# Kernel optimization log

Measured on AMD Instinct MI355X. Metric: run time of the kernel, lower is better.

Reference implementation:

```python
import jax, jax.numpy as jnp
import numpy as np

T = 3.0  # distillation temperature (hardcoded in AED.__init__)


def setup_inputs() -> dict:
    key = jax.random.key(0)
    ks = jax.random.split(key, 5)
    B, C = 1024, 32000
    return {
        "outputs1": jax.random.normal(ks[0], (B, C), dtype=jnp.float32),
        "outputs2": jax.random.normal(ks[1], (B, C), dtype=jnp.float32),
        "outputs3": jax.random.normal(ks[2], (B, C), dtype=jnp.float32),
        "outputs4": jax.random.normal(ks[3], (B, C), dtype=jnp.float32),
        "targets": jax.random.randint(ks[4], (B,), 0, C, dtype=jnp.int64),
    }


def reference(outputs1, outputs2, outputs3, outputs4, targets):
    # outs: [4, B, C]
    outs = jnp.stack([outputs1, outputs2, outputs3, outputs4], axis=0)
    mimic = jnp.mean(outs, axis=0)  # [B, C]
    C = outs.shape[-1]

    # Per-model CE loss: -log_softmax(logits)[target]  -> [4, B]
    logp = jax.nn.log_softmax(outs, axis=-1)
    CE = -jnp.take_along_axis(logp, targets[None, :, None], axis=2)[..., 0]

    # KD loss: KLDivLoss(reduction='mean') * T^2 = mean_c p_t*(log p_t - log p_s) * T^2
    teacher = 0.8 * outs + 0.2 * mimic[None]          # [4, B, C]
    log_s = jax.nn.log_softmax(outs / T, axis=-1)
    log_t = jax.nn.log_softmax(teacher / T, axis=-1)
    p_t = jnp.exp(log_t)
    KD = jnp.mean(p_t * (log_t - log_s), axis=-1) * (T * T)  # [4, B]

    Loss_IRM = jnp.sum(CE + KD, axis=0)  # [B]
    min_CE = jnp.min(CE, axis=0)         # argmin-based select == min

    # Deleting the target entry from each logit vector before the cosine is
    # equivalent (for dot products and norms) to zeroing that entry.
    tgt_mask = jax.nn.one_hot(targets, C, dtype=outs.dtype)  # [B, C]
    om = outs * (1.0 - tgt_mask[None])                        # [4, B, C]
    norms = jnp.sqrt(jnp.sum(om * om, axis=-1))               # [4, B]
    dots = jnp.einsum('jbc,kbc->jkb', om, om)                 # [4, 4, B]
    cos = dots / (norms[:, None, :] * norms[None, :, :])
    ju, ku = jnp.triu_indices(4, k=1)
    Loss_DAL = jnp.sum(cos[ju, ku], axis=0)  # [B], sum over 6 pairs j<k

    L = Loss_IRM + 0.7 * min_CE + 0.3 * Loss_DAL  # [B]
    return jnp.mean(L), mimic
```

## Files before the change

### kernel.cpp

```cpp
#include <hip/hip_runtime.h>
#include <math.h>


#define CCOLS 32000
#define VCOLS (CCOLS / 4)
#define BLOCK 512
#define NWAVES (BLOCK / 64)
#define NACC 26

__device__ __forceinline__ float wred(float v) {
#pragma unroll
  for (int o = 32; o > 0; o >>= 1) v += __shfl_down(v, o, 64);
  return v;
}

__global__ __launch_bounds__(BLOCK, 8) void aed_row(
    const float* __restrict__ x0, const float* __restrict__ x1,
    const float* __restrict__ x2, const float* __restrict__ x3,
    const int* __restrict__ tgt, float* __restrict__ out,
    float* __restrict__ rowloss) {
  const int b = blockIdx.x;
  const size_t off = (size_t)b * CCOLS;
  const float4* p0 = (const float4*)(x0 + off);
  const float4* p1 = (const float4*)(x1 + off);
  const float4* p2 = (const float4*)(x2 + off);
  const float4* p3 = (const float4*)(x3 + off);
  float* mim = out + 1 + off;

  float acc[NACC];
#pragma unroll
  for (int i = 0; i < NACC; ++i) acc[i] = 0.f;

  const float c1 = 0.48089835f;
  const float c08 = 0.38471868f;
  const float c02 = 0.09617967f;

  for (int v = threadIdx.x; v < VCOLS; v += BLOCK) {
    float4 A = p0[v];
    float4 B = p1[v];
    float4 Cc = p2[v];
    float4 D = p3[v];
    float a0[4] = {A.x, A.y, A.z, A.w};
    float a1[4] = {B.x, B.y, B.z, B.w};
    float a2[4] = {Cc.x, Cc.y, Cc.z, Cc.w};
    float a3[4] = {D.x, D.y, D.z, D.w};
#pragma unroll
    for (int u = 0; u < 4; ++u) {
      float y0 = a0[u], y1 = a1[u], y2 = a2[u], y3 = a3[u];
      float m = 0.25f * ((y0 + y1) + (y2 + y3));
      mim[4 * v + u] = m;
      float mm = m * c02;
#define MODEL(j, y)                                       \
  {                                                       \
    float t1 = __builtin_amdgcn_exp2f((y)*c1);            \
    acc[4 + (j)] += t1;                                   \
    acc[0 + (j)] += t1 * t1 * t1;                         \
    float e = __builtin_amdgcn_exp2f(fmaf((y), c08, mm)); \
    acc[8 + (j)] += e;                                    \
    acc[12 + (j)] = fmaf(e, m - (y), acc[12 + (j)]);      \
  }
      MODEL(0, y0)
      MODEL(1, y1)
      MODEL(2, y2)
      MODEL(3, y3)
#undef MODEL
      acc[16] = fmaf(y0, y0, acc[16]);
      acc[17] = fmaf(y1, y1, acc[17]);
      acc[18] = fmaf(y2, y2, acc[18]);
      acc[19] = fmaf(y3, y3, acc[19]);
      acc[20] = fmaf(y0, y1, acc[20]);
      acc[21] = fmaf(y0, y2, acc[21]);
      acc[22] = fmaf(y0, y3, acc[22]);
      acc[23] = fmaf(y1, y2, acc[23]);
      acc[24] = fmaf(y1, y3, acc[24]);
      acc[25] = fmaf(y2, y3, acc[25]);
    }
  }

  __shared__ float sm[NWAVES][NACC];
  const int lane = threadIdx.x & 63;
  const int wid = threadIdx.x >> 6;
#pragma unroll
  for (int i = 0; i < NACC; ++i) {
    float r = wred(acc[i]);
    if (lane == 0) sm[wid][i] = r;
  }
  __syncthreads();

  if (threadIdx.x == 0) {
    float t[NACC];
#pragma unroll
    for (int i = 0; i < NACC; ++i) {
      float s = 0.f;
#pragma unroll
      for (int w = 0; w < NWAVES; ++w) s += sm[w][i];
      t[i] = s;
    }

    const int tg = tgt[b];
    float tv[4];
    tv[0] = x0[off + tg];
    tv[1] = x1[off + tg];
    tv[2] = x2[off + tg];
    tv[3] = x3[off + tg];

    float CE[4], KD[4];
#pragma unroll
    for (int j = 0; j < 4; ++j) {
      CE[j] = logf(t[0 + j]) - tv[j];
      float LS = logf(t[4 + j]);
      float LT = logf(t[8 + j]);
      float S = t[12 + j] / t[8 + j];
      KD[j] = (9.f / 32000.f) * fmaf(0.2f / 3.f, S, LS - LT);
    }

    float n[4];
#pragma unroll
    for (int j = 0; j < 4; ++j) n[j] = sqrtf(t[16 + j] - tv[j] * tv[j]);

    float DAL = 0.f;
    DAL += (t[20] - tv[0] * tv[1]) / (n[0] * n[1]);
    DAL += (t[21] - tv[0] * tv[2]) / (n[0] * n[2]);
    DAL += (t[22] - tv[0] * tv[3]) / (n[0] * n[3]);
    DAL += (t[23] - tv[1] * tv[2]) / (n[1] * n[2]);
    DAL += (t[24] - tv[1] * tv[3]) / (n[1] * n[3]);
    DAL += (t[25] - tv[2] * tv[3]) / (n[2] * n[3]);

    float IRM = 0.f, mce = CE[0];
#pragma unroll
    for (int j = 0; j < 4; ++j) {
      IRM += CE[j] + KD[j];
      mce = fminf(mce, CE[j]);
    }
    rowloss[b] = IRM + 0.7f * mce + 0.3f * DAL;
  }
}

__global__ __launch_bounds__(256) void aed_final(const float* __restrict__ rowloss,
                                                 float* __restrict__ out, int B) {
  float v = 0.f;
  for (int i = threadIdx.x; i < B; i += 256) v += rowloss[i];
  __shared__ float sm[4];
  v = wred(v);
  if ((threadIdx.x & 63) == 0) sm[threadIdx.x >> 6] = v;
  __syncthreads();
  if (threadIdx.x == 0)
    out[0] = ((sm[0] + sm[1]) + (sm[2] + sm[3])) / (float)B;
}

extern "C" void kernel_launch(void* const* d_in, const int* in_sizes, int n_in,
                              void* d_out, int out_size, void* d_ws, size_t ws_size,
                              hipStream_t stream) {
  const float* o1 = (const float*)d_in[0];
  const float* o2 = (const float*)d_in[1];
  const float* o3 = (const float*)d_in[2];
  const float* o4 = (const float*)d_in[3];
  const int* tg = (const int*)d_in[4];
  float* out = (float*)d_out;
  float* ws = (float*)d_ws;
  const int B = in_sizes[4];

  aed_row<<<B, BLOCK, 0, stream>>>(o1, o2, o3, o4, tg, out, ws);
  aed_final<<<1, 256, 0, stream>>>(ws, out, B);
}
```

Baseline: 604.8 us.

## Split each row across two smaller blocks and move per-row finalize to final kernel

Result: faster. 513.5 us (-15.1%).

```diff
diff --git a/kernel.cpp b/kernel.cpp
--- a/kernel.cpp
+++ b/kernel.cpp
@@ -4,9 +4,11 @@
 
 #define CCOLS 32000
 #define VCOLS (CCOLS / 4)
-#define BLOCK 512
-#define NWAVES (BLOCK / 64)
+#define BLOCK 256
+#define SPLIT 2
+#define CHUNK (VCOLS / SPLIT)
 #define NACC 26
+#define WSTRIDE 32
 
 __device__ __forceinline__ float wred(float v) {
 #pragma unroll
@@ -14,12 +16,13 @@
   return v;
 }
 
-__global__ __launch_bounds__(BLOCK, 8) void aed_row(
+__global__ __launch_bounds__(BLOCK) void aed_row_part(
     const float* __restrict__ x0, const float* __restrict__ x1,
     const float* __restrict__ x2, const float* __restrict__ x3,
-    const int* __restrict__ tgt, float* __restrict__ out,
-    float* __restrict__ rowloss) {
-  const int b = blockIdx.x;
+    float* __restrict__ out, float* __restrict__ ws) {
+  const int bs = blockIdx.x;
+  const int b = bs >> 1;
+  const int s = bs & 1;
   const size_t off = (size_t)b * CCOLS;
   const float4* p0 = (const float4*)(x0 + off);
   const float4* p1 = (const float4*)(x1 + off);
@@ -35,7 +38,8 @@
   const float c08 = 0.38471868f;
   const float c02 = 0.09617967f;
 
-  for (int v = threadIdx.x; v < VCOLS; v += BLOCK) {
+  const int vend = (s + 1) * CHUNK;
+  for (int v = s * CHUNK + threadIdx.x; v < vend; v += BLOCK) {
     float4 A = p0[v];
     float4 B = p1[v];
     float4 Cc = p2[v];
@@ -48,7 +52,7 @@
     for (int u = 0; u < 4; ++u) {
       float y0 = a0[u], y1 = a1[u], y2 = a2[u], y3 = a3[u];
       float m = 0.25f * ((y0 + y1) + (y2 + y3));
-      mim[4 * v + u] = m;
+      __builtin_nontemporal_store(m, mim + 4 * v + u);
       float mm = m * c02;
 #define MODEL(j, y)                                       \
   {                                                       \
@@ -77,7 +81,7 @@
     }
   }
 
-  __shared__ float sm[NWAVES][NACC];
+  __shared__ float sm[4][NACC];
   const int lane = threadIdx.x & 63;
   const int wid = threadIdx.x >> 6;
 #pragma unroll
@@ -87,16 +91,27 @@
   }
   __syncthreads();
 
-  if (threadIdx.x == 0) {
+  if (threadIdx.x < NACC) {
+    const int i = threadIdx.x;
+    ws[(size_t)bs * WSTRIDE + i] =
+        ((sm[0][i] + sm[1][i]) + (sm[2][i] + sm[3][i]));
+  }
+}
+
+__global__ __launch_bounds__(1024) void aed_finalize(
+    const float* __restrict__ x0, const float* __restrict__ x1,
+    const float* __restrict__ x2, const float* __restrict__ x3,
+    const int* __restrict__ tgt, const float* __restrict__ ws,
+    float* __restrict__ out, int B) {
+  float L = 0.f;
+  for (int b = threadIdx.x; b < B; b += 1024) {
     float t[NACC];
+    const float* w0 = ws + (size_t)(2 * b) * WSTRIDE;
+    const float* w1 = w0 + WSTRIDE;
 #pragma unroll
-    for (int i = 0; i < NACC; ++i) {
-      float s = 0.f;
-#pragma unroll
-      for (int w = 0; w < NWAVES; ++w) s += sm[w][i];
-      t[i] = s;
-    }
+    for (int i = 0; i < NACC; ++i) t[i] = w0[i] + w1[i];
 
+    const size_t off = (size_t)b * CCOLS;
     const int tg = tgt[b];
     float tv[4];
     tv[0] = x0[off + tg];
@@ -132,20 +147,19 @@
       IRM += CE[j] + KD[j];
       mce = fminf(mce, CE[j]);
     }
-    rowloss[b] = IRM + 0.7f * mce + 0.3f * DAL;
+    L += IRM + 0.7f * mce + 0.3f * DAL;
   }
-}
 
-__global__ __launch_bounds__(256) void aed_final(const float* __restrict__ rowloss,
-                                                 float* __restrict__ out, int B) {
-  float v = 0.f;
-  for (int i = threadIdx.x; i < B; i += 256) v += rowloss[i];
-  __shared__ float sm[4];
-  v = wred(v);
-  if ((threadIdx.x & 63) == 0) sm[threadIdx.x >> 6] = v;
+  __shared__ float sm[16];
+  float r = wred(L);
+  if ((threadIdx.x & 63) == 0) sm[threadIdx.x >> 6] = r;
   __syncthreads();
-  if (threadIdx.x == 0)
-    out[0] = ((sm[0] + sm[1]) + (sm[2] + sm[3])) / (float)B;
+  if (threadIdx.x == 0) {
+    float s = 0.f;
+#pragma unroll
+    for (int w = 0; w < 16; ++w) s += sm[w];
+    out[0] = s / (float)B;
+  }
 }
 
 extern "C" void kernel_launch(void* const* d_in, const int* in_sizes, int n_in,
@@ -160,6 +174,6 @@
   float* ws = (float*)d_ws;
   const int B = in_sizes[4];
 
-  aed_row<<<B, BLOCK, 0, stream>>>(o1, o2, o3, o4, tg, out, ws);
-  aed_final<<<1, 256, 0, stream>>>(ws, out, B);
+  aed_row_part<<<B * SPLIT, BLOCK, 0, stream>>>(o1, o2, o3, o4, out, ws);
+  aed_finalize<<<1, 1024, 0, stream>>>(o1, o2, o3, o4, tg, ws, out, B);
 }
```
